# Performance work log

Measured on AMD Instinct MI355X. Metric: run time of the kernel, lower is better.

Reference implementation:

```python
import jax, jax.numpy as jnp
import numpy as np

N = 32768        # number of sum nodes in this partition
E = 32           # children (edges) per node, padded to power of 2
B = 256          # batch size
MAX_ELS = 65536  # ch_prod_layer_size
NUM_PARAMS = N * E


def setup_inputs() -> dict:
    key = jax.random.key(0)
    k1, k2, k3, k4, k5 = jax.random.split(key, 5)
    node_mars = jax.random.normal(k1, (N, B), dtype=jnp.float32)
    element_mars = jax.random.normal(k2, (MAX_ELS, B), dtype=jnp.float32)
    params = jax.random.uniform(k3, (NUM_PARAMS,), dtype=jnp.float32)  # nonneg mixture weights
    nids = jnp.arange(N, dtype=jnp.int32)                                # unique scatter targets
    cids = jax.random.randint(k4, (N, E), 0, MAX_ELS, dtype=jnp.int32)
    pids = jax.random.randint(k5, (N, E), 0, NUM_PARAMS, dtype=jnp.int32)
    return {"node_mars": node_mars, "element_mars": element_mars, "params": params,
            "nids": nids, "cids": cids, "pids": pids}


def reference(node_mars, element_mars, params, nids, cids, pids):
    # Gather child log-marginals: [N, E, B]
    ch_mars = element_mars[cids]
    # Numerically-stabilized weighted logsumexp over children (dim=1)
    maxval = jnp.max(ch_mars, axis=1, keepdims=True)                 # [N, 1, B]
    w = params[pids][:, :, None]                                     # [N, E, 1]
    s = jnp.sum(jnp.exp(ch_mars - maxval) * w, axis=1)               # [N, B]
    vals = jnp.log(jnp.clip(s, 1e-10, None)) + jnp.squeeze(maxval, 1)
    # Scatter into node_mars
    return node_mars.at[nids].set(vals)
```

## Files before the change

kernel.cpp:

```cpp
#include <hip/hip_runtime.h>
#include <hip/hip_fp16.h>
#include <hip/hip_fp8.h>


constexpr int NN = 32768;
constexpr int EE = 32;
constexpr int BB = 256;
constexpr int MAX_ELS = 65536;
constexpr int NODES_PER_BLOCK = 4;

typedef float floatx2 __attribute__((ext_vector_type(2)));

__device__ inline int pack4_fp8(float4 v) {
    const int a = __hip_cvt_float_to_fp8(__expf(v.x), __HIP_SATFINITE, __HIP_E4M3);
    const int b = __hip_cvt_float_to_fp8(__expf(v.y), __HIP_SATFINITE, __HIP_E4M3);
    const int c = __hip_cvt_float_to_fp8(__expf(v.z), __HIP_SATFINITE, __HIP_E4M3);
    const int d = __hip_cvt_float_to_fp8(__expf(v.w), __HIP_SATFINITE, __HIP_E4M3);
    return a | (b << 8) | (c << 16) | (d << 24);
}

__global__ __launch_bounds__(256)
void exp_convert_kernel(const float4* __restrict__ em, int4* __restrict__ G)
{
    const int i = blockIdx.x * 256 + threadIdx.x;
    const float4 v0 = em[4*i+0], v1 = em[4*i+1], v2 = em[4*i+2], v3 = em[4*i+3];
    int4 o;
    o.x = pack4_fp8(v0);
    o.y = pack4_fp8(v1);
    o.z = pack4_fp8(v2);
    o.w = pack4_fp8(v3);
    G[i] = o;
}

__global__ __launch_bounds__(256)
void pack_kernel(const float* __restrict__ params, const int* __restrict__ pids,
                 const int* __restrict__ cids, unsigned int* __restrict__ P)
{
    const int i = blockIdx.x * 256 + threadIdx.x;
    const unsigned int cid = (unsigned int)cids[i];
    const unsigned short wb = __half_as_ushort(__float2half(params[pids[i]]));
    P[i] = cid | ((unsigned int)wb << 16);
}

__global__ __launch_bounds__(256)
void sum_main_kernel(const unsigned int* __restrict__ G,
                     const unsigned int* __restrict__ P,
                     const int* __restrict__ nids,
                     float* __restrict__ out)
{
    const int tid  = threadIdx.x;
    const int wave = tid >> 6;
    const int lane = tid & 63;

    __shared__ unsigned int s_pack[NODES_PER_BLOCK][EE];
    if (tid < NODES_PER_BLOCK * EE) {
        s_pack[tid >> 5][tid & 31] = P[blockIdx.x * (NODES_PER_BLOCK * EE) + tid];
    }
    __syncthreads();

    float4 acc = make_float4(0.f, 0.f, 0.f, 0.f);
#pragma unroll
    for (int e = 0; e < EE; ++e) {
        const unsigned int pk = s_pack[wave][e];
        const unsigned int row = pk & 0xFFFFu;
        const float w = __half2float(__ushort_as_half((unsigned short)(pk >> 16)));
        const unsigned int u = G[(size_t)row * 64 + lane];
        const floatx2 lo = __builtin_amdgcn_cvt_pk_f32_fp8(u, false);
        const floatx2 hi = __builtin_amdgcn_cvt_pk_f32_fp8(u, true);
        acc.x = fmaf(lo.x, w, acc.x);
        acc.y = fmaf(lo.y, w, acc.y);
        acc.z = fmaf(hi.x, w, acc.z);
        acc.w = fmaf(hi.y, w, acc.w);
    }

    float4 r;
    r.x = __logf(fmaxf(acc.x, 1e-10f));
    r.y = __logf(fmaxf(acc.y, 1e-10f));
    r.z = __logf(fmaxf(acc.z, 1e-10f));
    r.w = __logf(fmaxf(acc.w, 1e-10f));

    const int n = blockIdx.x * NODES_PER_BLOCK + wave;
    *reinterpret_cast<float4*>(out + (size_t)nids[n] * BB + 4 * lane) = r;
}

__global__ __launch_bounds__(256, 2)
void sum_layer_fallback(const float* __restrict__ element_mars,
                        const float* __restrict__ params,
                        const int* __restrict__ nids,
                        const int* __restrict__ cids,
                        const int* __restrict__ pids,
                        float* __restrict__ out)
{
    const int tid  = threadIdx.x;
    const int wave = tid >> 6;
    const int lane = tid & 63;

    __shared__ int   s_cid[NODES_PER_BLOCK][EE];
    __shared__ float s_w[NODES_PER_BLOCK][EE];
    if (tid < NODES_PER_BLOCK * EE) {
        const int wi = tid >> 5, e = tid & (EE - 1);
        const int gn = blockIdx.x * NODES_PER_BLOCK + wi;
        s_cid[wi][e] = cids[gn * EE + e];
        s_w[wi][e]   = params[pids[gn * EE + e]];
    }
    __syncthreads();

    const int n = blockIdx.x * NODES_PER_BLOCK + wave;
    float4 acc = make_float4(0.f, 0.f, 0.f, 0.f);
#pragma unroll
    for (int e = 0; e < EE; ++e) {
        const float4 v = *reinterpret_cast<const float4*>(
            element_mars + (size_t)s_cid[wave][e] * BB + 4 * lane);
        const float w = s_w[wave][e];
        acc.x = fmaf(__expf(v.x), w, acc.x);
        acc.y = fmaf(__expf(v.y), w, acc.y);
        acc.z = fmaf(__expf(v.z), w, acc.z);
        acc.w = fmaf(__expf(v.w), w, acc.w);
    }
    float4 r;
    r.x = __logf(fmaxf(acc.x, 1e-10f));
    r.y = __logf(fmaxf(acc.y, 1e-10f));
    r.z = __logf(fmaxf(acc.z, 1e-10f));
    r.w = __logf(fmaxf(acc.w, 1e-10f));
    *reinterpret_cast<float4*>(out + (size_t)nids[n] * BB + 4 * lane) = r;
}

extern "C" void kernel_launch(void* const* d_in, const int* in_sizes, int n_in,
                              void* d_out, int out_size, void* d_ws, size_t ws_size,
                              hipStream_t stream) {
    const float* element_mars = (const float*)d_in[1];
    const float* params       = (const float*)d_in[2];
    const int*   nids         = (const int*)d_in[3];
    const int*   cids         = (const int*)d_in[4];
    const int*   pids         = (const int*)d_in[5];
    float*       out          = (float*)d_out;

    const size_t g_bytes = (size_t)MAX_ELS * BB;
    const size_t p_bytes = (size_t)NN * EE * sizeof(unsigned int);

    if (ws_size >= g_bytes + p_bytes) {
        unsigned int* G = (unsigned int*)d_ws;
        unsigned int* P = (unsigned int*)((char*)d_ws + g_bytes);

        exp_convert_kernel<<<(MAX_ELS * BB / 16) / 256, 256, 0, stream>>>(
            (const float4*)element_mars, (int4*)G);
        pack_kernel<<<(NN * EE) / 256, 256, 0, stream>>>(params, pids, cids, P);
        sum_main_kernel<<<NN / NODES_PER_BLOCK, 256, 0, stream>>>(
            G, P, nids, out);
    } else {
        sum_layer_fallback<<<NN / NODES_PER_BLOCK, 256, 0, stream>>>(
            element_mars, params, nids, cids, pids, out);
    }
}
```

Measured before the change: 177.1 us.

## Split fp8 table into batch slices pinned to XCDs via atomic work queue

```diff
diff --git a/kernel.cpp b/kernel.cpp
--- a/kernel.cpp
+++ b/kernel.cpp
@@ -7,29 +7,38 @@
 constexpr int EE = 32;
 constexpr int BB = 256;
 constexpr int MAX_ELS = 65536;
-constexpr int NODES_PER_BLOCK = 4;
+constexpr int SLICES = 8;
+constexpr int NODES_PER_CHUNK = 16;
+constexpr int NCHUNK = NN / NODES_PER_CHUNK;
+constexpr int TOTAL_ITEMS = SLICES * NCHUNK;
+constexpr int SLICE_U32 = MAX_ELS * 8;
 
 typedef float floatx2 __attribute__((ext_vector_type(2)));
+typedef float floatx4 __attribute__((ext_vector_type(4)));
+typedef unsigned int uintx2 __attribute__((ext_vector_type(2)));
 
-__device__ inline int pack4_fp8(float4 v) {
-    const int a = __hip_cvt_float_to_fp8(__expf(v.x), __HIP_SATFINITE, __HIP_E4M3);
-    const int b = __hip_cvt_float_to_fp8(__expf(v.y), __HIP_SATFINITE, __HIP_E4M3);
-    const int c = __hip_cvt_float_to_fp8(__expf(v.z), __HIP_SATFINITE, __HIP_E4M3);
-    const int d = __hip_cvt_float_to_fp8(__expf(v.w), __HIP_SATFINITE, __HIP_E4M3);
+__device__ inline unsigned int pack4_fp8exp(float4 v) {
+    const unsigned int a = __hip_cvt_float_to_fp8(__expf(v.x), __HIP_SATFINITE, __HIP_E4M3);
+    const unsigned int b = __hip_cvt_float_to_fp8(__expf(v.y), __HIP_SATFINITE, __HIP_E4M3);
+    const unsigned int c = __hip_cvt_float_to_fp8(__expf(v.z), __HIP_SATFINITE, __HIP_E4M3);
+    const unsigned int d = __hip_cvt_float_to_fp8(__expf(v.w), __HIP_SATFINITE, __HIP_E4M3);
     return a | (b << 8) | (c << 16) | (d << 24);
 }
 
+__global__ void zero_ctrs_kernel(int* __restrict__ ctr) {
+    if (threadIdx.x < 16) ctr[threadIdx.x] = 0;
+}
+
 __global__ __launch_bounds__(256)
-void exp_convert_kernel(const float4* __restrict__ em, int4* __restrict__ G)
+void exp_convert_kernel(const float4* __restrict__ em, unsigned int* __restrict__ G)
 {
-    const int i = blockIdx.x * 256 + threadIdx.x;
-    const float4 v0 = em[4*i+0], v1 = em[4*i+1], v2 = em[4*i+2], v3 = em[4*i+3];
-    int4 o;
-    o.x = pack4_fp8(v0);
-    o.y = pack4_fp8(v1);
-    o.z = pack4_fp8(v2);
-    o.w = pack4_fp8(v3);
-    G[i] = o;
+    const int i  = blockIdx.x * 256 + threadIdx.x;
+    const int r  = i >> 6;
+    const int cq = i & 63;
+    const float4 v = em[i];
+    const int s  = cq >> 3;
+    const int qq = cq & 7;
+    G[s * SLICE_U32 + r * 8 + qq] = pack4_fp8exp(v);
 }
 
 __global__ __launch_bounds__(256)
@@ -46,41 +55,75 @@
 void sum_main_kernel(const unsigned int* __restrict__ G,
                      const unsigned int* __restrict__ P,
                      const int* __restrict__ nids,
+                     int* __restrict__ ctr,
                      float* __restrict__ out)
 {
-    const int tid  = threadIdx.x;
-    const int wave = tid >> 6;
-    const int lane = tid & 63;
+    __shared__ int s_item;
+    __shared__ unsigned int s_pk[NODES_PER_CHUNK * EE];
 
-    __shared__ unsigned int s_pack[NODES_PER_BLOCK][EE];
-    if (tid < NODES_PER_BLOCK * EE) {
-        s_pack[tid >> 5][tid & 31] = P[blockIdx.x * (NODES_PER_BLOCK * EE) + tid];
+    if (threadIdx.x == 0) {
+        const int xcc = __builtin_amdgcn_s_getreg(6164) & (SLICES - 1);
+        int item = -1;
+        for (int a = 0; a < SLICES; ++a) {
+            const int s = (xcc + a) & (SLICES - 1);
+            const int c = atomicAdd(&ctr[s], 1);
+            if (c < NCHUNK) { item = s * NCHUNK + c; break; }
+        }
+        s_item = item;
     }
     __syncthreads();
+    const int item = s_item;
+    if (item < 0) return;
+    const int s = item >> 11;
+    const int c = item & (NCHUNK - 1);
 
-    float4 acc = make_float4(0.f, 0.f, 0.f, 0.f);
+    const int tid = threadIdx.x;
+    const int base_n = c * NODES_PER_CHUNK;
+
+    const uintx2 pv = __builtin_nontemporal_load(
+        (const uintx2*)(P + (size_t)base_n * EE) + tid);
+    s_pk[2 * tid]     = pv.x;
+    s_pk[2 * tid + 1] = pv.y;
+    __syncthreads();
+
+    const int wv = tid >> 6, lane = tid & 63;
+    const int g = lane >> 3;
+    const int q = lane & 7;
+    const unsigned int* Gs = G + (size_t)s * SLICE_U32;
+
+    for (int j = 0; j < 4; ++j) {
+        const int nl = wv * 4 + j;
+        float4 acc = make_float4(0.f, 0.f, 0.f, 0.f);
 #pragma unroll
-    for (int e = 0; e < EE; ++e) {
-        const unsigned int pk = s_pack[wave][e];
-        const unsigned int row = pk & 0xFFFFu;
-        const float w = __half2float(__ushort_as_half((unsigned short)(pk >> 16)));
-        const unsigned int u = G[(size_t)row * 64 + lane];
-        const floatx2 lo = __builtin_amdgcn_cvt_pk_f32_fp8(u, false);
-        const floatx2 hi = __builtin_amdgcn_cvt_pk_f32_fp8(u, true);
-        acc.x = fmaf(lo.x, w, acc.x);
-        acc.y = fmaf(lo.y, w, acc.y);
-        acc.z = fmaf(hi.x, w, acc.z);
-        acc.w = fmaf(hi.y, w, acc.w);
+        for (int k = 0; k < 4; ++k) {
+            const unsigned int pk = s_pk[nl * EE + k * 8 + g];
+            const float w = __half2float(__ushort_as_half((unsigned short)(pk >> 16)));
+            const unsigned int u = Gs[(size_t)(pk & 0xFFFFu) * 8 + q];
+            const floatx2 lo = __builtin_amdgcn_cvt_pk_f32_fp8(u, false);
+            const floatx2 hi = __builtin_amdgcn_cvt_pk_f32_fp8(u, true);
+            acc.x = fmaf(lo.x, w, acc.x);
+            acc.y = fmaf(lo.y, w, acc.y);
+            acc.z = fmaf(hi.x, w, acc.z);
+            acc.w = fmaf(hi.y, w, acc.w);
+        }
+#pragma unroll
+        for (int m = 8; m <= 32; m <<= 1) {
+            acc.x += __shfl_xor(acc.x, m);
+            acc.y += __shfl_xor(acc.y, m);
+            acc.z += __shfl_xor(acc.z, m);
+            acc.w += __shfl_xor(acc.w, m);
+        }
+        if (g == 0) {
+            const int n = base_n + nl;
+            floatx4 r;
+            r.x = __logf(fmaxf(acc.x, 1e-10f));
+            r.y = __logf(fmaxf(acc.y, 1e-10f));
+            r.z = __logf(fmaxf(acc.z, 1e-10f));
+            r.w = __logf(fmaxf(acc.w, 1e-10f));
+            __builtin_nontemporal_store(r,
+                (floatx4*)(out + (size_t)nids[n] * BB + s * 32) + q);
+        }
     }
-
-    float4 r;
-    r.x = __logf(fmaxf(acc.x, 1e-10f));
-    r.y = __logf(fmaxf(acc.y, 1e-10f));
-    r.z = __logf(fmaxf(acc.z, 1e-10f));
-    r.w = __logf(fmaxf(acc.w, 1e-10f));
-
-    const int n = blockIdx.x * NODES_PER_BLOCK + wave;
-    *reinterpret_cast<float4*>(out + (size_t)nids[n] * BB + 4 * lane) = r;
 }
 
 __global__ __launch_bounds__(256, 2)
@@ -95,17 +138,17 @@
     const int wave = tid >> 6;
     const int lane = tid & 63;
 
-    __shared__ int   s_cid[NODES_PER_BLOCK][EE];
-    __shared__ float s_w[NODES_PER_BLOCK][EE];
-    if (tid < NODES_PER_BLOCK * EE) {
+    __shared__ int   s_cid[4][EE];
+    __shared__ float s_w[4][EE];
+    if (tid < 4 * EE) {
         const int wi = tid >> 5, e = tid & (EE - 1);
-        const int gn = blockIdx.x * NODES_PER_BLOCK + wi;
+        const int gn = blockIdx.x * 4 + wi;
         s_cid[wi][e] = cids[gn * EE + e];
         s_w[wi][e]   = params[pids[gn * EE + e]];
     }
     __syncthreads();
 
-    const int n = blockIdx.x * NODES_PER_BLOCK + wave;
+    const int n = blockIdx.x * 4 + wave;
     float4 acc = make_float4(0.f, 0.f, 0.f, 0.f);
 #pragma unroll
     for (int e = 0; e < EE; ++e) {
@@ -137,18 +180,20 @@
 
     const size_t g_bytes = (size_t)MAX_ELS * BB;
     const size_t p_bytes = (size_t)NN * EE * sizeof(unsigned int);
+    const size_t c_bytes = 64;
 
-    if (ws_size >= g_bytes + p_bytes) {
+    if (ws_size >= g_bytes + p_bytes + c_bytes) {
         unsigned int* G = (unsigned int*)d_ws;
         unsigned int* P = (unsigned int*)((char*)d_ws + g_bytes);
+        int*        ctr = (int*)((char*)d_ws + g_bytes + p_bytes);
 
-        exp_convert_kernel<<<(MAX_ELS * BB / 16) / 256, 256, 0, stream>>>(
-            (const float4*)element_mars, (int4*)G);
+        zero_ctrs_kernel<<<1, 64, 0, stream>>>(ctr);
+        exp_convert_kernel<<<(MAX_ELS * 64) / 256, 256, 0, stream>>>(
+            (const float4*)element_mars, G);
         pack_kernel<<<(NN * EE) / 256, 256, 0, stream>>>(params, pids, cids, P);
-        sum_main_kernel<<<NN / NODES_PER_BLOCK, 256, 0, stream>>>(
-            G, P, nids, out);
+        sum_main_kernel<<<TOTAL_ITEMS, 256, 0, stream>>>(G, P, nids, ctr, out);
     } else {
-        sum_layer_fallback<<<NN / NODES_PER_BLOCK, 256, 0, stream>>>(
+        sum_layer_fallback<<<NN / 4, 256, 0, stream>>>(
             element_mars, params, nids, cids, pids, out);
     }
 }
```

Result: slower. 339.7 us (+91.8%).
